# Kernel optimization log

Measured on AMD Instinct MI355X. Metric: run time of the kernel, lower is better.

The kernel has to match this reference:

```python
import jax, jax.numpy as jnp
import numpy as np

H = 32      # num_attention_heads
HD = 64     # head_dim
MD = 64     # qk_mqa_dim (rope dim)
EPS = 1e-6
SCALING = (HD + MD) ** -0.5
NEG = -1e9


def rms_norm(x, w):
    var = jnp.mean(jnp.square(x), axis=-1, keepdims=True)
    return x * jax.lax.rsqrt(var + EPS) * w


def rotate_half(x):
    x1, x2 = jnp.split(x, 2, axis=-1)
    return jnp.concatenate([-x2, x1], axis=-1)


def apply_rope(x, cos, sin):
    return x * cos + rotate_half(x) * sin


def setup_inputs() -> dict:
    key = jax.random.key(0)
    ks = jax.random.split(key, 6)
    B, S, D = 1, 2048, 2048
    QR, KVR = 1024, 896
    hidden_states = jax.random.normal(ks[0], (B, S, D), jnp.float32)
    # real rotary tables for the MD-dim rope subspace
    inv_freq = 1.0 / (10000.0 ** (np.arange(0, MD, 2, dtype=np.float32) / MD))
    freqs = np.arange(S, dtype=np.float32)[:, None] * inv_freq[None, :]
    emb = np.concatenate([freqs, freqs], axis=-1)  # [S, MD]
    cos = jnp.asarray(np.cos(emb), jnp.float32)
    sin = jnp.asarray(np.sin(emb), jnp.float32)
    s = 0.02
    Wqa = jax.random.normal(ks[1], (QR, D), jnp.float32) * s
    q_ln_w = jnp.ones((QR,), jnp.float32)
    Wqb = jax.random.normal(ks[2], (H * (HD + MD), QR), jnp.float32) * s
    Wkva = jax.random.normal(ks[3], (KVR + MD, D), jnp.float32) * s
    kv_ln_w = jnp.ones((KVR,), jnp.float32)
    Wkvb = jax.random.normal(ks[4], (2 * H * HD, KVR), jnp.float32) * s
    Wo = jax.random.normal(ks[5], (D, H * HD), jnp.float32) * s
    return {"hidden_states": hidden_states, "cos": cos, "sin": sin,
            "Wqa": Wqa, "q_ln_w": q_ln_w, "Wqb": Wqb,
            "Wkva": Wkva, "kv_ln_w": kv_ln_w, "Wkvb": Wkvb, "Wo": Wo}


def reference(hidden_states, cos, sin, Wqa, q_ln_w, Wqb, Wkva, kv_ln_w, Wkvb, Wo):
    B, S, D = hidden_states.shape
    KVR = kv_ln_w.shape[0]
    # Q: LoRA down -> RMSNorm -> up (weights pre-absorbed with rope split)
    q = rms_norm(hidden_states @ Wqa.T, q_ln_w) @ Wqb.T      # [B,S,H*(HD+MD)]
    q = q.reshape(B, S, H, HD + MD).transpose(0, 2, 1, 3)     # [B,H,S,HD+MD]
    q_nope, q_rope = q[..., :HD], q[..., HD:]
    # KV: shared compressed latent + MQA rope key
    ckv = hidden_states @ Wkva.T                               # [B,S,KVR+MD]
    kv_nope, k_rope = ckv[..., :KVR], ckv[..., KVR:]
    kv_nope = rms_norm(kv_nope, kv_ln_w)
    q_rope = apply_rope(q_rope, cos[None, None], sin[None, None])
    k_rope = apply_rope(k_rope[:, None], cos[None, None], sin[None, None])  # [B,1,S,MD]
    # up-project latent to per-head K_nope and V (interleaved per head)
    kv = (kv_nope @ Wkvb.T).reshape(B, S, H, 2 * HD).transpose(0, 2, 1, 3)  # [B,H,S,2*HD]
    k_nope, value = kv[..., :HD], kv[..., HD:]
    key_states = jnp.concatenate(
        [k_nope, jnp.broadcast_to(k_rope, (B, H, S, MD))], axis=-1)  # repeat_kv of rope part
    query_states = jnp.concatenate([q_nope, q_rope], axis=-1)        # [B,H,S,HD+MD]
    # causal SDPA with scaling = (head_dim + qk_mqa_dim)^-0.5
    scores = jnp.einsum('bhqd,bhkd->bhqk', query_states, key_states) * SCALING
    causal = jnp.tril(jnp.ones((S, S), bool))
    scores = jnp.where(causal[None, None], scores, NEG)
    probs = jax.nn.softmax(scores, axis=-1)
    out = jnp.einsum('bhqk,bhkd->bhqd', probs, value)                # [B,H,S,HD]
    out = out.transpose(0, 2, 1, 3).reshape(B, S, H * HD)
    return out @ Wo.T
```

## Files before the change

kernel.cpp:

```cpp
#include <hip/hip_runtime.h>
#include <stdint.h>

typedef unsigned short u16;
typedef __attribute__((ext_vector_type(4))) float f32x4;
typedef __attribute__((ext_vector_type(4))) unsigned short u16x4;
typedef __attribute__((ext_vector_type(8))) unsigned short u16x8;
typedef __attribute__((ext_vector_type(8))) short s16x8;
typedef __attribute__((ext_vector_type(4))) short s16x4;
typedef __attribute__((ext_vector_type(2))) unsigned int u32x2;

#define DEVI static __device__ __forceinline__

#define VMCNT(n) asm volatile("s_waitcnt vmcnt(" #n ")" ::: "memory")
#define SBAR() __builtin_amdgcn_s_barrier()
#define SCHED0() __builtin_amdgcn_sched_barrier(0)

DEVI u16 f2b(float f) {
  union { float f; unsigned u; } v; v.f = f;
  unsigned r = v.u + 0x7fffu + ((v.u >> 16) & 1u);
  return (u16)(r >> 16);
}
DEVI float b2f(u16 b) {
  union { unsigned u; float f; } v; v.u = ((unsigned)b) << 16;
  return v.f;
}

DEVI void gload_lds16(const void* gptr, void* lptr) {
  typedef const __attribute__((address_space(1))) unsigned gq;
  typedef __attribute__((address_space(3))) unsigned lq;
  __builtin_amdgcn_global_load_lds((gq*)(uintptr_t)gptr,
                                   (lq*)(uint32_t)(uintptr_t)lptr, 16, 0, 0);
}

DEVI unsigned cvtpk(float a, float b) {
  unsigned d;
  asm("v_cvt_pk_bf16_f32 %0, %1, %2" : "=v"(d) : "v"(a), "v"(b));
  return d;
}
DEVI f32x4 mfma16(s16x4 a, s16x4 b, f32x4 c) {
  f32x4 d;
  asm("v_mfma_f32_16x16x16_bf16 %0, %1, %2, %3" : "=v"(d) : "v"(a), "v"(b), "v"(c));
  return d;
}
DEVI float exp2a(float x) {
  float d;
  asm("v_exp_f32 %0, %1" : "=v"(d) : "v"(x));
  return d;
}

__global__ __launch_bounds__(256) void cvt_all(
    const float* __restrict__ X, const float* __restrict__ Wqa,
    const float* __restrict__ Wkva, const float* __restrict__ Wqb,
    const float* __restrict__ Wkvb, const float* __restrict__ Wo,
    u16* __restrict__ Xb, u16* __restrict__ W1, u16* __restrict__ Wqbb,
    u16* __restrict__ Wkvbb, u16* __restrict__ Wob) {
  int i = blockIdx.x * 256 + threadIdx.x;
  const int stride = gridDim.x * 256;
  for (; i < 5079040; i += stride) {
    const float* s; u16* d; int j;
    if (i < 1572864) {
      if (i < 1048576) { s = X; d = Xb; j = i; }
      else             { s = Wqa; d = W1; j = i - 1048576; }
    } else if (i < 3112960) {
      if (i < 2064384) { s = Wkva; d = W1 + 1024 * 2048; j = i - 1572864; }
      else             { s = Wqb; d = Wqbb; j = i - 2064384; }
    } else {
      if (i < 4030464) { s = Wkvb; d = Wkvbb; j = i - 3112960; }
      else             { s = Wo; d = Wob; j = i - 4030464; }
    }
    f32x4 v = *(const f32x4*)(s + (size_t)j * 4);
    u16x4 o;
    o[0] = f2b(v[0]); o[1] = f2b(v[1]); o[2] = f2b(v[2]); o[3] = f2b(v[3]);
    *(u16x4*)(d + (size_t)j * 4) = o;
  }
}

#define GEMM_STAGE(AP, BP, KK, k0, buf)                                        \
  {                                                                            \
    _Pragma("unroll") for (int p = 0; p < 4; ++p) {                            \
      const int c = tid + p * 256;                                             \
      const int row = c >> 3, j = c & 7;                                       \
      gload_lds16(AP + (size_t)(m0 + row) * (KK) + (k0) + ((j ^ (row & 7)) * 8), \
                  &As[buf][c * 8]);                                            \
    }                                                                          \
    _Pragma("unroll") for (int p = 0; p < 4; ++p) {                            \
      const int c = tid + p * 256;                                             \
      const int row = c >> 3, j = c & 7;                                       \
      gload_lds16(BP + (size_t)(n0 + row) * (KK) + (k0) + ((j ^ (row & 7)) * 8), \
                  &Bs[buf][c * 8]);                                            \
    }                                                                          \
  }

#define GEMM_COMPUTE(cur)                                                      \
  _Pragma("unroll") for (int kk = 0; kk < 64; kk += 32) {                      \
    s16x8 af[4], bfr[4];                                                       \
    _Pragma("unroll") for (int i = 0; i < 4; ++i) {                            \
      const int rA = wm * 64 + i * 16 + c15;                                   \
      af[i] = *(const s16x8*)((const char*)&As[cur][0] + rA * 128 +            \
                              (((kk + g * 8) * 2) ^ ((rA & 7) << 4)));         \
    }                                                                          \
    _Pragma("unroll") for (int i = 0; i < 4; ++i) {                            \
      const int rB = wn * 64 + i * 16 + c15;                                   \
      bfr[i] = *(const s16x8*)((const char*)&Bs[cur][0] + rB * 128 +           \
                               (((kk + g * 8) * 2) ^ ((rB & 7) << 4)));        \
    }                                                                          \
    _Pragma("unroll") for (int i = 0; i < 4; ++i)                              \
      _Pragma("unroll") for (int j = 0; j < 4; ++j)                            \
        acc[i][j] = __builtin_amdgcn_mfma_f32_16x16x32_bf16(af[i], bfr[j],     \
                                                            acc[i][j], 0, 0, 0); \
  }

#define GEMM_PROLOG                                                            \
  const int tid = threadIdx.x;                                                 \
  const int lane = tid & 63, w = tid >> 6;                                     \
  const int wm = w >> 1, wn = w & 1;                                           \
  const int c15 = lane & 15, g = lane >> 4;                                    \
  const int m0 = blockIdx.y * 128, n0 = blockIdx.x * 128;                      \
  f32x4 acc[4][4] = {};

#define GEMM_LOOP(AP, BP, KK)                                                  \
  GEMM_STAGE(AP, BP, KK, 0, 0);                                                \
  const int nk = (KK) >> 6;                                                    \
  for (int kt = 0; kt < nk; ++kt) {                                            \
    const int cur = kt & 1;                                                    \
    if (kt + 1 < nk) {                                                         \
      GEMM_STAGE(AP, BP, KK, (kt + 1) << 6, cur ^ 1);                          \
      VMCNT(8);                                                                \
    } else {                                                                   \
      VMCNT(0);                                                                \
    }                                                                          \
    SBAR(); SCHED0();                                                          \
    GEMM_COMPUTE(cur);                                                         \
    SBAR(); SCHED0();                                                          \
  }

#define GEMM_LOOP3(AP, BP, KK)                                                 \
  GEMM_STAGE(AP, BP, KK, 0, 0);                                                \
  GEMM_STAGE(AP, BP, KK, 64, 1);                                               \
  const int nk = (KK) >> 6;                                                    \
  int bufc = 0;                                                                \
  for (int kt = 0; kt < nk; ++kt) {                                            \
    const int nxt = (bufc + 2 >= 3) ? bufc - 1 : bufc + 2;                     \
    if (kt + 2 < nk) {                                                         \
      GEMM_STAGE(AP, BP, KK, (kt + 2) << 6, nxt);                              \
      VMCNT(16);                                                               \
    } else if (kt + 1 < nk) {                                                  \
      VMCNT(8);                                                                \
    } else {                                                                   \
      VMCNT(0);                                                                \
    }                                                                          \
    SBAR(); SCHED0();                                                          \
    GEMM_COMPUTE(bufc);                                                        \
    SBAR(); SCHED0();                                                          \
    bufc = (bufc + 1 == 3) ? 0 : bufc + 1;                                     \
  }

template <int OUT_BF16>
__global__ __launch_bounds__(256) void gemm_out(const u16* __restrict__ A,
                                                const u16* __restrict__ B,
                                                void* __restrict__ Cv,
                                                int M, int N, int K) {
  __shared__ __align__(16) u16 As[3][128 * 64];
  __shared__ __align__(16) u16 Bs[3][128 * 64];
  GEMM_PROLOG
  GEMM_LOOP3(A, B, K)
#pragma unroll
  for (int i = 0; i < 4; ++i)
#pragma unroll
    for (int j = 0; j < 4; ++j) {
      const int mr = m0 + wm * 64 + i * 16 + g * 4;
      const int nc = n0 + wn * 64 + j * 16 + c15;
#pragma unroll
      for (int r = 0; r < 4; ++r) {
        if (OUT_BF16)
          ((u16*)Cv)[(size_t)(mr + r) * N + nc] = f2b(acc[i][j][r]);
        else
          ((float*)Cv)[(size_t)(mr + r) * N + nc] = acc[i][j][r];
      }
    }
}

__global__ __launch_bounds__(256) void gemm2_fused(
    const u16* __restrict__ qn, const u16* __restrict__ Wqbb,
    const u16* __restrict__ kvn, const u16* __restrict__ Wkvbb,
    u16* __restrict__ qraw, char* __restrict__ KbB, char* __restrict__ VtB) {
  __shared__ __align__(16) u16 As[2][128 * 64];
  __shared__ __align__(16) u16 Bs[2][128 * 64];
  const int z = blockIdx.z;
  const u16* A = z ? kvn : qn;
  const u16* B = z ? Wkvbb : Wqbb;
  const int K = z ? 896 : 1024;
  GEMM_PROLOG
  GEMM_LOOP(A, B, K)

  if (z == 0) {
#pragma unroll
    for (int i = 0; i < 4; ++i)
#pragma unroll
      for (int j = 0; j < 4; ++j) {
        const int mr = m0 + wm * 64 + i * 16 + g * 4;
        const int nc = n0 + wn * 64 + j * 16 + c15;
#pragma unroll
        for (int r = 0; r < 4; ++r)
          qraw[(size_t)(mr + r) * 4096 + nc] = f2b(acc[i][j][r]);
      }
  } else {
    const int h = n0 >> 7;
#pragma unroll
    for (int i = 0; i < 4; ++i)
#pragma unroll
      for (int j = 0; j < 4; ++j) {
        const int mr = m0 + wm * 64 + i * 16 + g * 4;
        if (wn == 0) {
          const int d = j * 16 + c15;
#pragma unroll
          for (int r = 0; r < 4; ++r) {
            const int s = mr + r;
            *(u16*)(KbB + ((size_t)(h * 2048 + s) << 8) +
                    ((2 * d) ^ ((s & 7) << 4))) = f2b(acc[i][j][r]);
          }
        } else {
          const int d = j * 16 + c15;
          u16x4 o;
#pragma unroll
          for (int r = 0; r < 4; ++r) o[r] = f2b(acc[i][j][r]);
          *(u16x4*)(VtB + ((size_t)(h * 64 + d) << 12) +
                    ((2 * mr) ^ ((d & 7) << 4))) = o;
        }
      }
  }
}

DEVI float block_sum(float v, float* sbuf, int tid) {
#pragma unroll
  for (int o = 32; o; o >>= 1) v += __shfl_xor(v, o, 64);
  __syncthreads();
  if ((tid & 63) == 0) sbuf[tid >> 6] = v;
  __syncthreads();
  return sbuf[0] + sbuf[1] + sbuf[2] + sbuf[3];
}

__global__ __launch_bounds__(256) void norm_rope(const u16* __restrict__ C1b,
    const float* __restrict__ qw, const float* __restrict__ kw,
    const float* __restrict__ cosb, const float* __restrict__ sinb,
    u16* __restrict__ qn, u16* __restrict__ kvn, char* __restrict__ KbB) {
  __shared__ float sbuf[4];
  __shared__ __align__(16) u16 rv[64];
  const int s = blockIdx.x, tid = threadIdx.x;
  const u16* row = C1b + (size_t)s * 2048;

  u16x4 qv4 = *(const u16x4*)(row + tid * 4);
  float q0 = b2f(qv4[0]), q1 = b2f(qv4[1]), q2 = b2f(qv4[2]), q3 = b2f(qv4[3]);
  float ss = q0*q0 + q1*q1 + q2*q2 + q3*q3;
  ss = block_sum(ss, sbuf, tid);
  const float scale = rsqrtf(ss * (1.f / 1024.f) + 1e-6f);
  {
    f32x4 wv = *(const f32x4*)(qw + tid * 4);
    u16x4 o;
    o[0] = f2b(q0 * scale * wv[0]); o[1] = f2b(q1 * scale * wv[1]);
    o[2] = f2b(q2 * scale * wv[2]); o[3] = f2b(q3 * scale * wv[3]);
    *(u16x4*)(qn + (size_t)s * 1024 + tid * 4) = o;
  }

  float ss2 = 0.f;
  float k0 = 0, k1 = 0, k2 = 0, k3 = 0;
  if (tid < 224) {
    u16x4 kv4 = *(const u16x4*)(row + 1024 + tid * 4);
    k0 = b2f(kv4[0]); k1 = b2f(kv4[1]); k2 = b2f(kv4[2]); k3 = b2f(kv4[3]);
    ss2 = k0*k0 + k1*k1 + k2*k2 + k3*k3;
  }
  ss2 = block_sum(ss2, sbuf, tid);
  const float sc2 = rsqrtf(ss2 * (1.f / 896.f) + 1e-6f);
  if (tid < 224) {
    f32x4 wv = *(const f32x4*)(kw + tid * 4);
    u16x4 o;
    o[0] = f2b(k0 * sc2 * wv[0]); o[1] = f2b(k1 * sc2 * wv[1]);
    o[2] = f2b(k2 * sc2 * wv[2]); o[3] = f2b(k3 * sc2 * wv[3]);
    *(u16x4*)(kvn + (size_t)s * 896 + tid * 4) = o;
  }

  if (tid < 64) {
    const int d = tid;
    const float x = b2f(row[1920 + d]);
    const float part = b2f(row[1920 + (d < 32 ? d + 32 : d - 32)]);
    const float cv = cosb[s * 64 + d], sv = sinb[s * 64 + d];
    rv[d] = f2b(d < 32 ? (x * cv - part * sv) : (x * cv + part * sv));
  }
  __syncthreads();
  {
    const int h = tid >> 3, c8 = tid & 7;
    const u16x8 v = *(const u16x8*)&rv[c8 * 8];
    *(u16x8*)(KbB + ((size_t)(h * 2048 + s) << 8) +
              ((128 + c8 * 16) ^ ((s & 7) << 4))) = v;
  }
}

__global__ __launch_bounds__(256) void attn_fwd(
    const u16* __restrict__ Qb, const u16* __restrict__ Kb,
    const u16* __restrict__ Vt, const float* __restrict__ cosb,
    const float* __restrict__ sinb, u16* __restrict__ O1, u16* __restrict__ O2,
    float* __restrict__ L1, float* __restrict__ L2) {
  __shared__ __align__(16) u16 Klds[2][64 * 128];
  __shared__ __align__(16) u16 Vlds[2][64 * 64];
  const int tid = threadIdx.x;
  const int lane = tid & 63, w = tid >> 6;
  const int c15 = lane & 15, g = lane >> 4;
  const int orig = blockIdx.x;
  const int xcd = orig & 7, l = orig >> 3;
  const int h = xcd * 4 + (l & 3);
  const int rem = l >> 2;
  const int half = rem & 1;
  const int qb = 15 - (rem >> 1);
  const int kvbase = half ? 64 * (qb + 1) : 0;
  u16* Oh = half ? O2 : O1;
  float* Lh = half ? L2 : L1;
  const int wmin = qb * 128 + w * 32;
  const int wmax = wmin + 31;
  const char* KbHB = (const char*)Kb + ((size_t)h << 19);
  const char* VtHB = (const char*)Vt + ((size_t)h << 18);
  const float SC2 = 0.12753860478587782f;

  s16x8 qf[2][4];
#pragma unroll
  for (int qa = 0; qa < 2; ++qa) {
    const int qrow = wmin + qa * 16 + c15;
    const u16* qp = Qb + (size_t)qrow * 4096 + h * 128;
    u16x8 x0 = *(const u16x8*)(qp + g * 8);
    u16x8 x1 = *(const u16x8*)(qp + 32 + g * 8);
    u16x8 x2 = *(const u16x8*)(qp + 64 + g * 8);
    u16x8 x3 = *(const u16x8*)(qp + 96 + g * 8);
    const float* cb = cosb + (size_t)qrow * 64 + g * 8;
    const float* sb = sinb + (size_t)qrow * 64 + g * 8;
#pragma unroll
    for (int i = 0; i < 8; ++i) {
      qf[qa][0][i] = (short)f2b(b2f(x0[i]) * SC2);
      qf[qa][1][i] = (short)f2b(b2f(x1[i]) * SC2);
      const float f2 = b2f(x2[i]), f3 = b2f(x3[i]);
      qf[qa][2][i] = (short)f2b((f2 * cb[i] - f3 * sb[i]) * SC2);
      qf[qa][3][i] = (short)f2b((f3 * cb[32 + i] + f2 * sb[32 + i]) * SC2);
    }
  }

  const int nt = qb + 1;
  auto STAGE = [&](int t, int buf) {
    const int kv0g = kvbase + (t << 6);
#pragma unroll
    for (int p = 0; p < 4; ++p) {
      const int c = tid + p * 256;
      gload_lds16(KbHB + ((size_t)(kv0g + (c >> 4)) << 8) + (c & 15) * 16,
                  (char*)Klds[buf] + c * 16);
    }
#pragma unroll
    for (int p = 0; p < 2; ++p) {
      const int c = tid + p * 256;
      gload_lds16(VtHB + ((size_t)(c >> 3) << 12) + 2 * kv0g + (c & 7) * 16,
                  (char*)Vlds[buf] + c * 16);
    }
  };

  f32x4 acc[2][4] = {};
  float m[2] = {-1e9f, -1e9f}, ssum[2] = {0.f, 0.f};

  STAGE(0, 0);

  for (int t = 0; t < nt; ++t) {
    const int cur = t & 1;
    const int kv0g = kvbase + (t << 6);
    if (t + 1 < nt) {
      STAGE(t + 1, cur ^ 1);
      VMCNT(6);
    } else {
      VMCNT(0);
    }
    SBAR();
    SCHED0();

    if (kv0g <= wmax) {
      const u16* Kc = Klds[cur];
      const u16* Vc = Vlds[cur];

      float pv[2][4][4];
      __builtin_amdgcn_s_setprio(1);
#pragma unroll
      for (int kvh = 0; kvh < 4; ++kvh) {
        s16x8 kf[4];
        const int rb = (kvh * 16 + c15) * 256;
#pragma unroll
        for (int d0 = 0; d0 < 4; ++d0)
          kf[d0] = *(const s16x8*)((const char*)Kc + rb +
                                   ((d0 * 64 + g * 16) ^ ((c15 & 7) << 4)));
#pragma unroll
        for (int qa = 0; qa < 2; ++qa) {
          f32x4 s4 = {};
#pragma unroll
          for (int d0 = 0; d0 < 4; ++d0)
            s4 = __builtin_amdgcn_mfma_f32_16x16x32_bf16(kf[d0], qf[qa][d0], s4, 0, 0, 0);
          pv[qa][kvh][0] = s4[0]; pv[qa][kvh][1] = s4[1];
          pv[qa][kvh][2] = s4[2]; pv[qa][kvh][3] = s4[3];
        }
      }
      __builtin_amdgcn_s_setprio(0);

      if (kv0g + 63 > wmin) {
#pragma unroll
        for (int qa = 0; qa < 2; ++qa) {
          const int qrow = wmin + qa * 16 + c15;
#pragma unroll
          for (int kvh = 0; kvh < 4; ++kvh)
#pragma unroll
            for (int r = 0; r < 4; ++r) {
              const int kv = kv0g + kvh * 16 + g * 4 + r;
              if (kv > qrow) pv[qa][kvh][r] = -1e9f;
            }
        }
      }

      s16x4 pB[2][4];
#pragma unroll
      for (int qa = 0; qa < 2; ++qa) {
        float pm = -1e9f;
#pragma unroll
        for (int kvh = 0; kvh < 4; ++kvh)
#pragma unroll
          for (int r = 0; r < 4; ++r) pm = fmaxf(pm, pv[qa][kvh][r]);
        pm = fmaxf(pm, __shfl_xor(pm, 16, 64));
        pm = fmaxf(pm, __shfl_xor(pm, 32, 64));
        if (!__all(pm - m[qa] <= 8.f)) {
          const float mnew = fmaxf(m[qa], pm);
          const float alpha = exp2a(m[qa] - mnew);
          ssum[qa] *= alpha;
#pragma unroll
          for (int dt = 0; dt < 4; ++dt) acc[qa][dt] *= alpha;
          m[qa] = mnew;
        }
#pragma unroll
        for (int kvh = 0; kvh < 4; ++kvh)
#pragma unroll
          for (int r = 0; r < 4; ++r) {
            const float p = exp2a(pv[qa][kvh][r] - m[qa]);
            pv[qa][kvh][r] = p;
            ssum[qa] += p;
          }
#pragma unroll
        for (int ks = 0; ks < 4; ++ks) {
          u32x2 pw;
          pw[0] = cvtpk(pv[qa][ks][0], pv[qa][ks][1]);
          pw[1] = cvtpk(pv[qa][ks][2], pv[qa][ks][3]);
          pB[qa][ks] = __builtin_bit_cast(s16x4, pw);
        }
      }

      __builtin_amdgcn_s_setprio(1);
#pragma unroll
      for (int dt = 0; dt < 4; ++dt) {
        const int rb2 = (dt * 16 + c15) * 128;
#pragma unroll
        for (int ks = 0; ks < 4; ++ks) {
          s16x4 vf = *(const s16x4*)((const char*)Vc + rb2 +
                                     ((ks * 32 + g * 8) ^ ((c15 & 7) << 4)));
          acc[0][dt] = mfma16(vf, pB[0][ks], acc[0][dt]);
          acc[1][dt] = mfma16(vf, pB[1][ks], acc[1][dt]);
        }
      }
      __builtin_amdgcn_s_setprio(0);
    }
    SBAR();
    SCHED0();
  }

#pragma unroll
  for (int qa = 0; qa < 2; ++qa) {
    float sv = ssum[qa];
    sv += __shfl_xor(sv, 16, 64);
    sv += __shfl_xor(sv, 32, 64);
    const float inv = (sv > 0.f) ? 1.f / sv : 0.f;
    const int qrow = wmin + qa * 16 + c15;
#pragma unroll
    for (int dt = 0; dt < 4; ++dt) {
      u16x4 o;
#pragma unroll
      for (int r = 0; r < 4; ++r) o[r] = f2b(acc[qa][dt][r] * inv);
      *(u16x4*)(Oh + (size_t)qrow * 2048 + h * 64 + dt * 16 + g * 4) = o;
    }
    if (g == 0)
      Lh[qrow * 32 + h] = (sv > 0.f) ? m[qa] + __log2f(sv) : -3.0e38f;
  }
}

__global__ __launch_bounds__(256) void attn_combine(
    const u16* __restrict__ O1, const u16* __restrict__ O2,
    const float* __restrict__ L1, const float* __restrict__ L2,
    u16* __restrict__ attnb) {
  const int idx = blockIdx.x * 256 + threadIdx.x;
  const int base = idx * 8;
  const int qh = base >> 6;
  const float l1 = L1[qh], l2 = L2[qh];
  const float Lm = fmaxf(l1, l2);
  const float w1 = exp2a(l1 - Lm), w2 = exp2a(l2 - Lm);
  const float inv = 1.f / (w1 + w2);
  u16x8 a = *(const u16x8*)(O1 + base);
  u16x8 b = *(const u16x8*)(O2 + base);
  u16x8 o;
#pragma unroll
  for (int i = 0; i < 8; ++i)
    o[i] = f2b((b2f(a[i]) * w1 + b2f(b[i]) * w2) * inv);
  *(u16x8*)(attnb + base) = o;
}

extern "C" void kernel_launch(void* const* d_in, const int* in_sizes, int n_in,
                              void* d_out, int out_size, void* d_ws, size_t ws_size,
                              hipStream_t stream) {
  const float* X    = (const float*)d_in[0];
  const float* cosb = (const float*)d_in[1];
  const float* sinb = (const float*)d_in[2];
  const float* Wqa  = (const float*)d_in[3];
  const float* qlnw = (const float*)d_in[4];
  const float* Wqb  = (const float*)d_in[5];
  const float* Wkva = (const float*)d_in[6];
  const float* klnw = (const float*)d_in[7];
  const float* Wkvb = (const float*)d_in[8];
  const float* Wo   = (const float*)d_in[9];
  float* out = (float*)d_out;
  char* ws = (char*)d_ws;

  u16*   Xb     = (u16*)(ws + 0);
  u16*   W1     = (u16*)(ws + 8388608);
  u16*   C1b    = (u16*)(ws + 16777216);
  u16*   qn     = (u16*)(ws + 33554432);
  u16*   kvn    = (u16*)(ws + 37748736);
  u16*   Wqbb   = (u16*)(ws + 41943040);
  u16*   Wkvbb  = (u16*)(ws + 50331648);
  u16*   qraw_b = (u16*)(ws + 0);
  u16*   Kb     = (u16*)(ws + 58720256);
  u16*   VtG    = (u16*)(ws + 75497472);
  u16*   attnb  = (u16*)(ws + 83886080);
  u16*   Wob    = (u16*)(ws + 92274688);
  float* L1buf  = (float*)(ws + 33554432);
  float* L2buf  = (float*)(ws + 33554432 + 262144);
  u16*   O1buf  = (u16*)(ws + 41943040);
  u16*   O2buf  = (u16*)(ws + 50331648);

  cvt_all<<<2048, 256, 0, stream>>>(X, Wqa, Wkva, Wqb, Wkvb, Wo,
                                    Xb, W1, Wqbb, Wkvbb, Wob);

  gemm_out<1><<<dim3(16, 16), 256, 0, stream>>>(Xb, W1, C1b, 2048, 2048, 2048);

  norm_rope<<<2048, 256, 0, stream>>>(C1b, qlnw, klnw, cosb, sinb, qn, kvn, (char*)Kb);

  gemm2_fused<<<dim3(32, 16, 2), 256, 0, stream>>>(qn, Wqbb, kvn, Wkvbb,
                                                   qraw_b, (char*)Kb, (char*)VtG);

  attn_fwd<<<1024, 256, 0, stream>>>(qraw_b, Kb, VtG, cosb, sinb,
                                     O1buf, O2buf, L1buf, L2buf);

  attn_combine<<<2048, 256, 0, stream>>>(O1buf, O2buf, L1buf, L2buf, attnb);

  gemm_out<0><<<dim3(16, 16), 256, 0, stream>>>(attnb, Wob, out, 2048, 2048, 2048);
}
```

Measured before the change: 175.9 us.

## Rebalance causal attention work: split only long query blocks, run short ones whole

Replaces the uniform two-way KV split of every query block with a lookup-table schedule. Short query blocks (rows 0-1023) now run as a single unsplit work item that writes straight to the final attention buffer. Only long blocks are split in two and merged by a combine kernel that now covers just the upper half of rows. This cuts the grid from 1024 to 768 blocks and halves the combine work. The rescale path also skips the cross-lane max shuffles unless some lane exceeds the threshold. The risks are that the hand-coded tables balance load poorly, and that the deferred shuffle changes when rescaling triggers.

New measurement: 179.1 us. Within noise of the previous version (+1.8%).

```diff
diff --git a/kernel.cpp b/kernel.cpp
--- a/kernel.cpp
+++ b/kernel.cpp
@@ -298,7 +298,8 @@
 __global__ __launch_bounds__(256) void attn_fwd(
     const u16* __restrict__ Qb, const u16* __restrict__ Kb,
     const u16* __restrict__ Vt, const float* __restrict__ cosb,
-    const float* __restrict__ sinb, u16* __restrict__ O1, u16* __restrict__ O2,
+    const float* __restrict__ sinb, u16* __restrict__ attnb,
+    u16* __restrict__ O1, u16* __restrict__ O2,
     float* __restrict__ L1, float* __restrict__ L2) {
   __shared__ __align__(16) u16 Klds[2][64 * 128];
   __shared__ __align__(16) u16 Vlds[2][64 * 64];
@@ -309,11 +310,13 @@
   const int xcd = orig & 7, l = orig >> 3;
   const int h = xcd * 4 + (l & 3);
   const int rem = l >> 2;
-  const int half = rem & 1;
-  const int qb = 15 - (rem >> 1);
-  const int kvbase = half ? 64 * (qb + 1) : 0;
-  u16* Oh = half ? O2 : O1;
-  float* Lh = half ? L2 : L1;
+  const unsigned long long Q0 = 0x4BABACDF5CD6EE7Full;
+  const unsigned long long Q1 = 0x99883210ull;
+  const unsigned long long HH = 0x44AA94019648ull;
+  const int qb = (int)((rem < 16 ? (Q0 >> (4 * rem)) : (Q1 >> (4 * (rem - 16)))) & 15);
+  const int mode = (int)((HH >> (2 * rem)) & 3);
+  const int nt = (mode == 2) ? (2 * qb + 2) : (qb + 1);
+  const int kvbase = (mode == 1) ? ((qb + 1) << 6) : 0;
   const int wmin = qb * 128 + w * 32;
   const int wmax = wmin + 31;
   const char* KbHB = (const char*)Kb + ((size_t)h << 19);
@@ -341,7 +344,6 @@
     }
   }
 
-  const int nt = qb + 1;
   auto STAGE = [&](int t, int buf) {
     const int kv0g = kvbase + (t << 6);
 #pragma unroll
@@ -418,14 +420,14 @@
       s16x4 pB[2][4];
 #pragma unroll
       for (int qa = 0; qa < 2; ++qa) {
-        float pm = -1e9f;
+        float pml = -1e9f;
 #pragma unroll
         for (int kvh = 0; kvh < 4; ++kvh)
 #pragma unroll
-          for (int r = 0; r < 4; ++r) pm = fmaxf(pm, pv[qa][kvh][r]);
-        pm = fmaxf(pm, __shfl_xor(pm, 16, 64));
-        pm = fmaxf(pm, __shfl_xor(pm, 32, 64));
-        if (!__all(pm - m[qa] <= 8.f)) {
+          for (int r = 0; r < 4; ++r) pml = fmaxf(pml, pv[qa][kvh][r]);
+        if (!__all(pml - m[qa] <= 8.f)) {
+          float pm = fmaxf(pml, __shfl_xor(pml, 16, 64));
+          pm = fmaxf(pm, __shfl_xor(pm, 32, 64));
           const float mnew = fmaxf(m[qa], pm);
           const float alpha = exp2a(m[qa] - mnew);
           ssum[qa] *= alpha;
@@ -475,15 +477,27 @@
     sv += __shfl_xor(sv, 32, 64);
     const float inv = (sv > 0.f) ? 1.f / sv : 0.f;
     const int qrow = wmin + qa * 16 + c15;
-#pragma unroll
-    for (int dt = 0; dt < 4; ++dt) {
-      u16x4 o;
-#pragma unroll
-      for (int r = 0; r < 4; ++r) o[r] = f2b(acc[qa][dt][r] * inv);
-      *(u16x4*)(Oh + (size_t)qrow * 2048 + h * 64 + dt * 16 + g * 4) = o;
-    }
-    if (g == 0)
-      Lh[qrow * 32 + h] = (sv > 0.f) ? m[qa] + __log2f(sv) : -3.0e38f;
+    if (mode == 2) {
+#pragma unroll
+      for (int dt = 0; dt < 4; ++dt) {
+        u16x4 o;
+#pragma unroll
+        for (int r = 0; r < 4; ++r) o[r] = f2b(acc[qa][dt][r] * inv);
+        *(u16x4*)(attnb + (size_t)qrow * 2048 + h * 64 + dt * 16 + g * 4) = o;
+      }
+    } else {
+      u16* Oh = mode ? O2 : O1;
+      float* Lh = mode ? L2 : L1;
+#pragma unroll
+      for (int dt = 0; dt < 4; ++dt) {
+        u16x4 o;
+#pragma unroll
+        for (int r = 0; r < 4; ++r) o[r] = f2b(acc[qa][dt][r] * inv);
+        *(u16x4*)(Oh + (size_t)qrow * 2048 + h * 64 + dt * 16 + g * 4) = o;
+      }
+      if (g == 0)
+        Lh[qrow * 32 + h] = (sv > 0.f) ? m[qa] + __log2f(sv) : -3.0e38f;
+    }
   }
 }
 
@@ -492,7 +506,7 @@
     const float* __restrict__ L1, const float* __restrict__ L2,
     u16* __restrict__ attnb) {
   const int idx = blockIdx.x * 256 + threadIdx.x;
-  const int base = idx * 8;
+  const int base = 2097152 + idx * 8;
   const int qh = base >> 6;
   const float l1 = L1[qh], l2 = L2[qh];
   const float Lm = fmaxf(l1, l2);
@@ -550,10 +564,10 @@
   gemm2_fused<<<dim3(32, 16, 2), 256, 0, stream>>>(qn, Wqbb, kvn, Wkvbb,
                                                    qraw_b, (char*)Kb, (char*)VtG);
 
-  attn_fwd<<<1024, 256, 0, stream>>>(qraw_b, Kb, VtG, cosb, sinb,
-                                     O1buf, O2buf, L1buf, L2buf);
-
-  attn_combine<<<2048, 256, 0, stream>>>(O1buf, O2buf, L1buf, L2buf, attnb);
+  attn_fwd<<<768, 256, 0, stream>>>(qraw_b, Kb, VtG, cosb, sinb,
+                                    attnb, O1buf, O2buf, L1buf, L2buf);
+
+  attn_combine<<<1024, 256, 0, stream>>>(O1buf, O2buf, L1buf, L2buf, attnb);
 
   gemm_out<0><<<dim3(16, 16), 256, 0, stream>>>(attnb, Wob, out, 2048, 2048, 2048);
 }
```
